# Kernel tuning notes

Hardware: AMD Instinct MI355X
Metric: run time of the kernel (lower is better)

The kernel has to match this reference:

```python
import jax, jax.numpy as jnp
import numpy as np

N = 100000
E = 1600000
DIN = 128
DOUT = 128
NUM_STEPS = 3


def setup_inputs() -> dict:
    key = jax.random.key(0)
    ks = jax.random.split(key, 12)
    stdv = 1.0 / np.sqrt(DOUT)
    xav = np.sqrt(6.0 / (2 * DOUT + DOUT))  # xavier_uniform for [DOUT, 2*DOUT]
    return {
        "input": jax.random.normal(ks[0], (N, DIN), dtype=jnp.float32),
        "edge_row": jax.random.randint(ks[1], (E,), 0, N, dtype=jnp.int32),
        "edge_col": jax.random.randint(ks[2], (E,), 0, N, dtype=jnp.int32),
        "edge_weight": jax.random.uniform(ks[3], (E,), dtype=jnp.float32),
        "weight": jax.random.uniform(ks[4], (DIN, DOUT), jnp.float32, -stdv, stdv),
        "bias": jax.random.uniform(ks[5], (DOUT,), jnp.float32, -stdv, stdv),
        "candidate_weight": jax.random.uniform(ks[6], (DOUT, DOUT), jnp.float32, -stdv, stdv),
        "ug_W": jax.random.uniform(ks[7], (DOUT, 2 * DOUT), jnp.float32, -xav, xav),
        "ug_b": jnp.zeros((DOUT,), jnp.float32),
        "rg_W": jax.random.uniform(ks[8], (DOUT, 2 * DOUT), jnp.float32, -xav, xav),
        "rg_b": jnp.zeros((DOUT,), jnp.float32),
    }


def reference(input, edge_row, edge_col, edge_weight, weight, bias,
              candidate_weight, ug_W, ug_b, rg_W, rg_b):
    n = input.shape[0]
    # h = input @ W + b
    h = input @ weight + bias
    for _ in range(NUM_STEPS):
        # spmm: m[dst] += w_e * h[src]
        msg = edge_weight[:, None] * h[edge_col]          # [E, DOUT]
        m = jax.ops.segment_sum(msg, edge_row, num_segments=n)  # [N, DOUT]
        g = jnp.concatenate([h, m], axis=1)               # [N, 2*DOUT]
        z = jax.nn.sigmoid(g @ ug_W.T + ug_b)
        r = jax.nn.sigmoid(g @ rg_W.T + rg_b)
        cand = jnp.tanh((r * h) @ candidate_weight)
        h = z * h + (1.0 - z) * cand
    return h
```

## Files before the change

### kernel.cpp

```cpp
#include <hip/hip_runtime.h>
#include <math.h>

#define NN 100000
#define EE 1600000
#define D 128
#define NB 782
#define SBLK 98
#define EPB 16384

typedef __attribute__((ext_vector_type(8))) short short8;
typedef __attribute__((ext_vector_type(4))) float floatx4;

static __device__ __forceinline__ unsigned short f2bf(float f) {
  unsigned int u = __builtin_bit_cast(unsigned int, f);
  u = (u + 0x7fff + ((u >> 16) & 1)) >> 16;
  return (unsigned short)u;
}
static __device__ __forceinline__ unsigned int pk2(float a, float b) {
  return (unsigned int)f2bf(a) | ((unsigned int)f2bf(b) << 16);
}
static __device__ __forceinline__ float bflo(unsigned int u) { return __builtin_bit_cast(float, u << 16); }
static __device__ __forceinline__ float bfhi(unsigned int u) { return __builtin_bit_cast(float, u & 0xffff0000u); }
static __device__ __forceinline__ float bf2f(unsigned short s) {
  return __builtin_bit_cast(float, (unsigned int)s << 16);
}
static __device__ __forceinline__ float sig_f(float x) { return 1.f / (1.f + __expf(-x)); }
static __device__ __forceinline__ float tanh_f(float x) {
  float e = __expf(2.f * x);
  return 1.f - 2.f / (e + 1.f);
}


__global__ __launch_bounds__(1024) void b_count(const int* __restrict__ erow, int* __restrict__ cnt_pb) {
  __shared__ int s[NB];
  const int tid = threadIdx.x;
  for (int b = tid; b < NB; b += 1024) s[b] = 0;
  __syncthreads();
  const int base = blockIdx.x * EPB;
#pragma unroll
  for (int i = 0; i < 16; ++i) {
    int idx = base + i * 1024 + tid;
    if (idx < EE) atomicAdd(&s[erow[idx] >> 7], 1);
  }
  __syncthreads();
  for (int b = tid; b < NB; b += 1024) cnt_pb[blockIdx.x * NB + b] = s[b];
}

__global__ __launch_bounds__(1024) void b_scan(const int* __restrict__ cnt_pb,
                                               int* __restrict__ base_pb, int* __restrict__ bucket_off) {
  __shared__ int s[1024];
  const int b = threadIdx.x;
  int tot = 0;
  if (b < NB) {
    for (int j = 0; j < SBLK; ++j) tot += cnt_pb[j * NB + b];
  }
  s[b] = tot;
  __syncthreads();
  for (int d = 1; d < 1024; d <<= 1) {
    int v = (b >= d) ? s[b - d] : 0;
    __syncthreads();
    s[b] += v;
    __syncthreads();
  }
  int excl = s[b] - tot;
  if (b < NB) {
    bucket_off[b] = excl;
    int run = excl;
    for (int j = 0; j < SBLK; ++j) { base_pb[j * NB + b] = run; run += cnt_pb[j * NB + b]; }
  }
  if (b == NB - 1) bucket_off[NB] = excl + tot;
}

__global__ __launch_bounds__(1024) void b_scatter(const int* __restrict__ erow, const int* __restrict__ ecol,
                                                  const float* __restrict__ ew,
                                                  const int* __restrict__ base_pb, int2* __restrict__ arena) {
  __shared__ int cur[NB];
  const int tid = threadIdx.x;
  for (int b = tid; b < NB; b += 1024) cur[b] = base_pb[blockIdx.x * NB + b];
  __syncthreads();
  const int base = blockIdx.x * EPB;
#pragma unroll
  for (int i = 0; i < 16; ++i) {
    int idx = base + i * 1024 + tid;
    if (idx < EE) {
      int r = erow[idx];
      int pos = atomicAdd(&cur[r >> 7], 1);
      int2 v;
      v.x = ecol[idx] | ((r & 127) << 24);
      v.y = __builtin_bit_cast(int, ew[idx]);
      arena[pos] = v;
    }
  }
}

__global__ __launch_bounds__(256) void b_sort(const int* __restrict__ bucket_off, const int2* __restrict__ arena,
                                              int2* __restrict__ edata, int* __restrict__ row_start) {
  __shared__ int rcnt[128];
  __shared__ int rcur[128];
  const int b = blockIdx.x;
  const int tid = threadIdx.x;
  const int lo = bucket_off[b], hi = bucket_off[b + 1];

  if (tid < 128) rcnt[tid] = 0;
  __syncthreads();
  for (int i = lo + tid; i < hi; i += 256) atomicAdd(&rcnt[(arena[i].x >> 24) & 127], 1);
  __syncthreads();
  int myc = (tid < 128) ? rcnt[tid] : 0;
  for (int d = 1; d < 128; d <<= 1) {
    int v = (tid < 128 && tid >= d) ? rcnt[tid - d] : 0;
    __syncthreads();
    if (tid < 128) rcnt[tid] += v;
    __syncthreads();
  }
  if (tid < 128) {
    int excl = rcnt[tid] - myc;
    rcur[tid] = lo + excl;
    int gr = b * 128 + tid;
    if (gr < NN) row_start[gr] = lo + excl;
  }
  if (b == NB - 1 && tid == 0) row_start[NN] = hi;
  __syncthreads();

  for (int i = lo + tid; i < hi; i += 256) {
    int2 v = arena[i];
    int rl = (v.x >> 24) & 127;
    int pos = atomicAdd(&rcur[rl], 1);
    int2 o;
    o.x = v.x & 0x00FFFFFF;
    o.y = v.y;
    edata[pos] = o;
  }
}

__global__ __launch_bounds__(64) void k_pack_zr(const float* __restrict__ ugW, const float* __restrict__ rgW,
                                                unsigned int* __restrict__ packZR) {
  int g = blockIdx.x;
  int nt = g >> 3, ks = g & 7;
  int lane = threadIdx.x;
  int o = nt * 16 + (lane & 15);
  int c0 = ks * 32 + (lane >> 4) * 8;
  const float* src = (o < 128 ? ugW + (size_t)o * 256 : rgW + (size_t)(o - 128) * 256) + c0;
  float4 f0 = ((const float4*)src)[0];
  float4 f1 = ((const float4*)src)[1];
  uint4 out;
  out.x = pk2(f0.x, f0.y);
  out.y = pk2(f0.z, f0.w);
  out.z = pk2(f1.x, f1.y);
  out.w = pk2(f1.z, f1.w);
  ((uint4*)packZR)[g * 64 + lane] = out;
}

__global__ __launch_bounds__(64) void k_pack_kn(const float* __restrict__ M, unsigned int* __restrict__ pack) {
  int g = blockIdx.x;
  int nt = g >> 2, ks = g & 3;
  int lane = threadIdx.x;
  int n = nt * 16 + (lane & 15);
  int k0 = ks * 32 + (lane >> 4) * 8;
  unsigned short v[8];
#pragma unroll
  for (int j = 0; j < 8; ++j) v[j] = f2bf(M[(size_t)(k0 + j) * 128 + n]);
  uint4 out;
  out.x = (unsigned int)v[0] | ((unsigned int)v[1] << 16);
  out.y = (unsigned int)v[2] | ((unsigned int)v[3] << 16);
  out.z = (unsigned int)v[4] | ((unsigned int)v[5] << 16);
  out.w = (unsigned int)v[6] | ((unsigned int)v[7] << 16);
  ((uint4*)pack)[g * 64 + lane] = out;
}

__global__ __launch_bounds__(256) void init_mfma(
    const float* __restrict__ X, const short* __restrict__ packW, const float* __restrict__ bias,
    unsigned short* __restrict__ h_bf) {
  __shared__ __align__(16) short sX[32 * 136];
  const int tid = threadIdx.x;
  const int row0 = blockIdx.x * 32;

  {
    int r = tid >> 3, ch = tid & 7;
    const float4* px = (const float4*)(X + (size_t)(row0 + r) * D + ch * 16);
    float4 f0 = px[0], f1 = px[1], f2 = px[2], f3 = px[3];
    uint4 o0, o1;
    o0.x = pk2(f0.x, f0.y); o0.y = pk2(f0.z, f0.w);
    o0.z = pk2(f1.x, f1.y); o0.w = pk2(f1.z, f1.w);
    o1.x = pk2(f2.x, f2.y); o1.y = pk2(f2.z, f2.w);
    o1.z = pk2(f3.x, f3.y); o1.w = pk2(f3.z, f3.w);
    *(uint4*)(sX + r * 136 + ch * 16) = o0;
    *(uint4*)(sX + r * 136 + ch * 16 + 8) = o1;
  }
  __syncthreads();

  const int wave = tid >> 6, lane = tid & 63;
  const int quad = lane >> 4, l15 = lane & 15;
  const int mh = wave & 1, nh = wave >> 1;
  const int mrow = mh * 16 + l15;

  floatx4 acc[4];
  const floatx4 zero4 = {0.f, 0.f, 0.f, 0.f};
#pragma unroll
  for (int t = 0; t < 4; ++t) acc[t] = zero4;

  const short8* pW = (const short8*)packW;
#pragma unroll
  for (int ks = 0; ks < 4; ++ks) {
    short8 a = *(const short8*)(sX + mrow * 136 + ks * 32 + quad * 8);
#pragma unroll
    for (int t = 0; t < 4; ++t) {
      short8 b = pW[((nh * 4 + t) * 4 + ks) * 64 + lane];
      acc[t] = __builtin_amdgcn_mfma_f32_16x16x32_bf16(a, b, acc[t], 0, 0, 0);
    }
  }

#pragma unroll
  for (int t = 0; t < 4; ++t) {
    int col = nh * 64 + t * 16 + l15;
    float bv = bias[col];
#pragma unroll
    for (int reg = 0; reg < 4; ++reg) {
      int row = mh * 16 + quad * 4 + reg;
      h_bf[(size_t)(row0 + row) * D + col] = f2bf(acc[t][reg] + bv);
    }
  }
}

__global__ __launch_bounds__(512, 8) void fused_step(
    const int* __restrict__ row_start, const int2* __restrict__ edata,
    const uint4* __restrict__ h4,
    const short* __restrict__ packZR, const short* __restrict__ packCW,
    const float* __restrict__ ugb, const float* __restrict__ rgb,
    unsigned short* __restrict__ h_bf_out, float* __restrict__ h_f32_out, int last) {
  __shared__ __align__(16) short sA[32 * 264];
  __shared__ __align__(16) short sRH[32 * 136];

  const int tid = threadIdx.x;
  const int row0 = blockIdx.x * 32;
  const int wave = tid >> 6, lane = tid & 63;
  const int sub = lane >> 4, li = lane & 15;

  {
    int r = tid >> 4, ch = tid & 15;
    *(uint4*)(sA + r * 264 + ch * 8) = h4[(size_t)(row0 + r) * 16 + ch];
  }

  {
    const int rbase = row0 + wave * 4;
    int rs[5];
#pragma unroll
    for (int j = 0; j < 5; ++j) rs[j] = row_start[rbase + j];

    for (int i = 0; i < 4; ++i) {
      const int s0 = rs[i], end = rs[i + 1];
      float acc[8];
#pragma unroll
      for (int j = 0; j < 8; ++j) acc[j] = 0.f;

      int kk = s0;
      for (; kk + 8 <= end; kk += 8) {
        int2 e0 = edata[kk + sub];
        int2 e1 = edata[kk + 4 + sub];
        uint4 h0 = h4[(size_t)e0.x * 16 + li];
        uint4 h1 = h4[(size_t)e1.x * 16 + li];
        float w0 = __builtin_bit_cast(float, e0.y);
        float w1 = __builtin_bit_cast(float, e1.y);
        acc[0] += w0 * bflo(h0.x); acc[1] += w0 * bfhi(h0.x);
        acc[2] += w0 * bflo(h0.y); acc[3] += w0 * bfhi(h0.y);
        acc[4] += w0 * bflo(h0.z); acc[5] += w0 * bfhi(h0.z);
        acc[6] += w0 * bflo(h0.w); acc[7] += w0 * bfhi(h0.w);
        acc[0] += w1 * bflo(h1.x); acc[1] += w1 * bfhi(h1.x);
        acc[2] += w1 * bflo(h1.y); acc[3] += w1 * bfhi(h1.y);
        acc[4] += w1 * bflo(h1.z); acc[5] += w1 * bfhi(h1.z);
        acc[6] += w1 * bflo(h1.w); acc[7] += w1 * bfhi(h1.w);
      }
      for (; kk < end; kk += 4) {
        int e = kk + sub;
        if (e < end) {
          int2 ed = edata[e];
          uint4 hv = h4[(size_t)ed.x * 16 + li];
          float w = __builtin_bit_cast(float, ed.y);
          acc[0] += w * bflo(hv.x); acc[1] += w * bfhi(hv.x);
          acc[2] += w * bflo(hv.y); acc[3] += w * bfhi(hv.y);
          acc[4] += w * bflo(hv.z); acc[5] += w * bfhi(hv.z);
          acc[6] += w * bflo(hv.w); acc[7] += w * bfhi(hv.w);
        }
      }

#pragma unroll
      for (int j = 0; j < 8; ++j) acc[j] += __shfl_xor(acc[j], 16, 64);
#pragma unroll
      for (int j = 0; j < 8; ++j) acc[j] += __shfl_xor(acc[j], 32, 64);

      if (sub == 0) {
        int rl = wave * 4 + i;
        uint4 o;
        o.x = pk2(acc[0], acc[1]);
        o.y = pk2(acc[2], acc[3]);
        o.z = pk2(acc[4], acc[5]);
        o.w = pk2(acc[6], acc[7]);
        *(uint4*)(sA + rl * 264 + 128 + li * 8) = o;
      }
    }
  }
  __syncthreads();

  const int quad = lane >> 4, l15 = lane & 15;
  const int mh = wave >> 2, nh = wave & 3;
  const int mrow = mh * 16 + l15;

  floatx4 accZ[2], accR[2];
  const floatx4 zero4 = {0.f, 0.f, 0.f, 0.f};
#pragma unroll
  for (int t = 0; t < 2; ++t) { accZ[t] = zero4; accR[t] = zero4; }

  const short8* pB = (const short8*)packZR;
#pragma unroll
  for (int ks = 0; ks < 8; ++ks) {
    short8 a = *(const short8*)(sA + mrow * 264 + ks * 32 + quad * 8);
#pragma unroll
    for (int t = 0; t < 2; ++t) {
      short8 bz = pB[((nh * 2 + t) * 8 + ks) * 64 + lane];
      accZ[t] = __builtin_amdgcn_mfma_f32_16x16x32_bf16(a, bz, accZ[t], 0, 0, 0);
      short8 br = pB[((8 + nh * 2 + t) * 8 + ks) * 64 + lane];
      accR[t] = __builtin_amdgcn_mfma_f32_16x16x32_bf16(a, br, accR[t], 0, 0, 0);
    }
  }

#pragma unroll
  for (int t = 0; t < 2; ++t) {
    int col = nh * 32 + t * 16 + l15;
    float zb = ugb[col], rb = rgb[col];
#pragma unroll
    for (int reg = 0; reg < 4; ++reg) {
      int row = mh * 16 + quad * 4 + reg;
      float z = sig_f(accZ[t][reg] + zb);
      float rr = sig_f(accR[t][reg] + rb);
      float hv = bf2f((unsigned short)sA[row * 264 + col]);
      sRH[row * 136 + col] = (short)f2bf(rr * hv);
      accZ[t][reg] = z;
    }
  }
  __syncthreads();

  floatx4 acc2[2];
#pragma unroll
  for (int t = 0; t < 2; ++t) acc2[t] = zero4;

  const short8* pC = (const short8*)packCW;
#pragma unroll
  for (int ks = 0; ks < 4; ++ks) {
    short8 a = *(const short8*)(sRH + mrow * 136 + ks * 32 + quad * 8);
#pragma unroll
    for (int t = 0; t < 2; ++t) {
      short8 b = pC[((nh * 2 + t) * 4 + ks) * 64 + lane];
      acc2[t] = __builtin_amdgcn_mfma_f32_16x16x32_bf16(a, b, acc2[t], 0, 0, 0);
    }
  }

#pragma unroll
  for (int t = 0; t < 2; ++t) {
    int col = nh * 32 + t * 16 + l15;
#pragma unroll
    for (int reg = 0; reg < 4; ++reg) {
      int row = mh * 16 + quad * 4 + reg;
      float cand = tanh_f(acc2[t][reg]);
      float z = accZ[t][reg];
      float hold = bf2f((unsigned short)sA[row * 264 + col]);
      float hn = z * hold + (1.f - z) * cand;
      size_t gi = (size_t)(row0 + row) * D + col;
      if (last) h_f32_out[gi] = hn;
      else h_bf_out[gi] = f2bf(hn);
    }
  }
}

extern "C" void kernel_launch(void* const* d_in, const int* in_sizes, int n_in,
                              void* d_out, int out_size, void* d_ws, size_t ws_size,
                              hipStream_t stream) {
  const float* input = (const float*)d_in[0];
  const int* erow    = (const int*)d_in[1];
  const int* ecol    = (const int*)d_in[2];
  const float* ew    = (const float*)d_in[3];
  const float* W     = (const float*)d_in[4];
  const float* bias  = (const float*)d_in[5];
  const float* CW    = (const float*)d_in[6];
  const float* ugW   = (const float*)d_in[7];
  const float* ugb   = (const float*)d_in[8];
  const float* rgW   = (const float*)d_in[9];
  const float* rgb   = (const float*)d_in[10];

  float* h_out = (float*)d_out;

  char* ws = (char*)d_ws;
  unsigned short* hA = (unsigned short*)ws;   ws += (size_t)NN * D * 2;
  unsigned short* hB = (unsigned short*)ws;   ws += (size_t)NN * D * 2;
  unsigned int* packZR = (unsigned int*)ws;   ws += 16 * 8 * 64 * 16;
  unsigned int* packCW = (unsigned int*)ws;   ws += 8 * 4 * 64 * 16;
  unsigned int* packW  = (unsigned int*)ws;   ws += 8 * 4 * 64 * 16;
  int2* arena    = (int2*)ws;                 ws += (size_t)EE * sizeof(int2);
  int2* edata    = (int2*)ws;                 ws += (size_t)EE * sizeof(int2);
  int* cnt_pb    = (int*)ws;                  ws += SBLK * NB * sizeof(int);
  int* base_pb   = (int*)ws;                  ws += SBLK * NB * sizeof(int);
  int* bucket_off= (int*)ws;                  ws += (NB + 1) * sizeof(int);
  int* row_start = (int*)ws;                  ws += (NN + 1) * sizeof(int);

  b_count<<<SBLK, 1024, 0, stream>>>(erow, cnt_pb);
  b_scan<<<1, 1024, 0, stream>>>(cnt_pb, base_pb, bucket_off);
  b_scatter<<<SBLK, 1024, 0, stream>>>(erow, ecol, ew, base_pb, arena);
  b_sort<<<NB, 256, 0, stream>>>(bucket_off, arena, edata, row_start);

  k_pack_zr<<<128, 64, 0, stream>>>(ugW, rgW, packZR);
  k_pack_kn<<<32, 64, 0, stream>>>(CW, packCW);
  k_pack_kn<<<32, 64, 0, stream>>>(W, packW);
  init_mfma<<<NN / 32, 256, 0, stream>>>(input, (const short*)packW, bias, hA);

  fused_step<<<NN / 32, 512, 0, stream>>>(row_start, edata, (const uint4*)hA,
                                          (const short*)packZR, (const short*)packCW,
                                          ugb, rgb, hB, h_out, 0);
  fused_step<<<NN / 32, 512, 0, stream>>>(row_start, edata, (const uint4*)hB,
                                          (const short*)packZR, (const short*)packCW,
                                          ugb, rgb, hA, h_out, 0);
  fused_step<<<NN / 32, 512, 0, stream>>>(row_start, edata, (const uint4*)hA,
                                          (const short*)packZR, (const short*)packCW,
                                          ugb, rgb, hB, h_out, 1);
}
```

Measured before the change: 529.4 us.

## Stage edge chunks in LDS, assign one row per quarter-wave, coalesce output stores

The SpMM gather now loads each block's contiguous edge range into shared memory in chunks, and each 16-lane group handles a single row, so no cross-lane shuffle reduction is needed. Output writes in init and fused_step go through shared memory and are stored as 16-byte coalesced rows instead of scattered 2-byte stores. The bucketing kernels use 256-thread blocks over 4x more blocks, and their count buffers are placed in the h workspace that is not yet used. The cost is extra barriers and the LDS reuse for sRH, and a row's edges are processed serially by 16 lanes, which hurts when degrees vary.

Result: no change. 530.3 us (+0.2%).

```diff
diff --git a/kernel.cpp b/kernel.cpp
--- a/kernel.cpp
+++ b/kernel.cpp
@@ -5,8 +5,9 @@
 #define EE 1600000
 #define D 128
 #define NB 782
-#define SBLK 98
-#define EPB 16384
+#define SBLK 392
+#define EPB 4096
+#define EMAX 2048
 
 typedef __attribute__((ext_vector_type(8))) short short8;
 typedef __attribute__((ext_vector_type(4))) float floatx4;
@@ -29,21 +30,27 @@
   float e = __expf(2.f * x);
   return 1.f - 2.f / (e + 1.f);
 }
-
-
-__global__ __launch_bounds__(1024) void b_count(const int* __restrict__ erow, int* __restrict__ cnt_pb) {
+static __device__ __forceinline__ void fma8(float* acc, float w, uint4 h) {
+  acc[0] += w * bflo(h.x); acc[1] += w * bfhi(h.x);
+  acc[2] += w * bflo(h.y); acc[3] += w * bfhi(h.y);
+  acc[4] += w * bflo(h.z); acc[5] += w * bfhi(h.z);
+  acc[6] += w * bflo(h.w); acc[7] += w * bfhi(h.w);
+}
+
+
+__global__ __launch_bounds__(256) void b_count(const int* __restrict__ erow, int* __restrict__ cnt_pb) {
   __shared__ int s[NB];
   const int tid = threadIdx.x;
-  for (int b = tid; b < NB; b += 1024) s[b] = 0;
+  for (int b = tid; b < NB; b += 256) s[b] = 0;
   __syncthreads();
   const int base = blockIdx.x * EPB;
 #pragma unroll
   for (int i = 0; i < 16; ++i) {
-    int idx = base + i * 1024 + tid;
+    int idx = base + i * 256 + tid;
     if (idx < EE) atomicAdd(&s[erow[idx] >> 7], 1);
   }
   __syncthreads();
-  for (int b = tid; b < NB; b += 1024) cnt_pb[blockIdx.x * NB + b] = s[b];
+  for (int b = tid; b < NB; b += 256) cnt_pb[blockIdx.x * NB + b] = s[b];
 }
 
 __global__ __launch_bounds__(1024) void b_scan(const int* __restrict__ cnt_pb,
@@ -71,17 +78,17 @@
   if (b == NB - 1) bucket_off[NB] = excl + tot;
 }
 
-__global__ __launch_bounds__(1024) void b_scatter(const int* __restrict__ erow, const int* __restrict__ ecol,
+__global__ __launch_bounds__(256) void b_scatter(const int* __restrict__ erow, const int* __restrict__ ecol,
                                                   const float* __restrict__ ew,
                                                   const int* __restrict__ base_pb, int2* __restrict__ arena) {
   __shared__ int cur[NB];
   const int tid = threadIdx.x;
-  for (int b = tid; b < NB; b += 1024) cur[b] = base_pb[blockIdx.x * NB + b];
+  for (int b = tid; b < NB; b += 256) cur[b] = base_pb[blockIdx.x * NB + b];
   __syncthreads();
   const int base = blockIdx.x * EPB;
 #pragma unroll
   for (int i = 0; i < 16; ++i) {
-    int idx = base + i * 1024 + tid;
+    int idx = base + i * 256 + tid;
     if (idx < EE) {
       int r = erow[idx];
       int pos = atomicAdd(&cur[r >> 7], 1);
@@ -209,6 +216,7 @@
     }
   }
 
+  __syncthreads();
 #pragma unroll
   for (int t = 0; t < 4; ++t) {
     int col = nh * 64 + t * 16 + l15;
@@ -216,8 +224,13 @@
 #pragma unroll
     for (int reg = 0; reg < 4; ++reg) {
       int row = mh * 16 + quad * 4 + reg;
-      h_bf[(size_t)(row0 + row) * D + col] = f2bf(acc[t][reg] + bv);
-    }
+      sX[row * 136 + col] = (short)f2bf(acc[t][reg] + bv);
+    }
+  }
+  __syncthreads();
+  for (int idx = tid; idx < 512; idx += 256) {
+    int r = idx >> 4, ch = idx & 15;
+    *(uint4*)(h_bf + (size_t)(row0 + r) * D + ch * 8) = *(uint4*)(sX + r * 136 + ch * 8);
   }
 }
 
@@ -228,7 +241,9 @@
     const float* __restrict__ ugb, const float* __restrict__ rgb,
     unsigned short* __restrict__ h_bf_out, float* __restrict__ h_f32_out, int last) {
   __shared__ __align__(16) short sA[32 * 264];
-  __shared__ __align__(16) short sRH[32 * 136];
+  __shared__ __align__(16) char sU[EMAX * 8];
+  int2* sE = (int2*)sU;
+  short* sRH = (short*)sU;
 
   const int tid = threadIdx.x;
   const int row0 = blockIdx.x * 32;
@@ -240,63 +255,46 @@
     *(uint4*)(sA + r * 264 + ch * 8) = h4[(size_t)(row0 + r) * 16 + ch];
   }
 
+  const int myrow = row0 + wave * 4 + sub;
+  const int rs0 = row_start[myrow];
+  const int rs1 = row_start[myrow + 1];
+  const int seg_lo = row_start[row0];
+  const int seg_hi = row_start[row0 + 32];
+
+  float acc[8];
+#pragma unroll
+  for (int j = 0; j < 8; ++j) acc[j] = 0.f;
+
+  for (int clo = seg_lo; clo < seg_hi; clo += EMAX) {
+    const int chi = min(clo + EMAX, seg_hi);
+    for (int i = clo + tid; i < chi; i += 512) sE[i - clo] = edata[i];
+    __syncthreads();
+
+    int kb = max(rs0, clo) - clo;
+    int ke = min(rs1, chi) - clo;
+    for (; kb + 2 <= ke; kb += 2) {
+      int2 e0 = sE[kb];
+      int2 e1 = sE[kb + 1];
+      uint4 h0 = h4[(size_t)e0.x * 16 + li];
+      uint4 h1 = h4[(size_t)e1.x * 16 + li];
+      fma8(acc, __builtin_bit_cast(float, e0.y), h0);
+      fma8(acc, __builtin_bit_cast(float, e1.y), h1);
+    }
+    if (kb < ke) {
+      int2 e0 = sE[kb];
+      uint4 h0 = h4[(size_t)e0.x * 16 + li];
+      fma8(acc, __builtin_bit_cast(float, e0.y), h0);
+    }
+    __syncthreads();
+  }
+
   {
-    const int rbase = row0 + wave * 4;
-    int rs[5];
-#pragma unroll
-    for (int j = 0; j < 5; ++j) rs[j] = row_start[rbase + j];
-
-    for (int i = 0; i < 4; ++i) {
-      const int s0 = rs[i], end = rs[i + 1];
-      float acc[8];
-#pragma unroll
-      for (int j = 0; j < 8; ++j) acc[j] = 0.f;
-
-      int kk = s0;
-      for (; kk + 8 <= end; kk += 8) {
-        int2 e0 = edata[kk + sub];
-        int2 e1 = edata[kk + 4 + sub];
-        uint4 h0 = h4[(size_t)e0.x * 16 + li];
-        uint4 h1 = h4[(size_t)e1.x * 16 + li];
-        float w0 = __builtin_bit_cast(float, e0.y);
-        float w1 = __builtin_bit_cast(float, e1.y);
-        acc[0] += w0 * bflo(h0.x); acc[1] += w0 * bfhi(h0.x);
-        acc[2] += w0 * bflo(h0.y); acc[3] += w0 * bfhi(h0.y);
-        acc[4] += w0 * bflo(h0.z); acc[5] += w0 * bfhi(h0.z);
-        acc[6] += w0 * bflo(h0.w); acc[7] += w0 * bfhi(h0.w);
-        acc[0] += w1 * bflo(h1.x); acc[1] += w1 * bfhi(h1.x);
-        acc[2] += w1 * bflo(h1.y); acc[3] += w1 * bfhi(h1.y);
-        acc[4] += w1 * bflo(h1.z); acc[5] += w1 * bfhi(h1.z);
-        acc[6] += w1 * bflo(h1.w); acc[7] += w1 * bfhi(h1.w);
-      }
-      for (; kk < end; kk += 4) {
-        int e = kk + sub;
-        if (e < end) {
-          int2 ed = edata[e];
-          uint4 hv = h4[(size_t)ed.x * 16 + li];
-          float w = __builtin_bit_cast(float, ed.y);
-          acc[0] += w * bflo(hv.x); acc[1] += w * bfhi(hv.x);
-          acc[2] += w * bflo(hv.y); acc[3] += w * bfhi(hv.y);
-          acc[4] += w * bflo(hv.z); acc[5] += w * bfhi(hv.z);
-          acc[6] += w * bflo(hv.w); acc[7] += w * bfhi(hv.w);
-        }
-      }
-
-#pragma unroll
-      for (int j = 0; j < 8; ++j) acc[j] += __shfl_xor(acc[j], 16, 64);
-#pragma unroll
-      for (int j = 0; j < 8; ++j) acc[j] += __shfl_xor(acc[j], 32, 64);
-
-      if (sub == 0) {
-        int rl = wave * 4 + i;
-        uint4 o;
-        o.x = pk2(acc[0], acc[1]);
-        o.y = pk2(acc[2], acc[3]);
-        o.z = pk2(acc[4], acc[5]);
-        o.w = pk2(acc[6], acc[7]);
-        *(uint4*)(sA + rl * 264 + 128 + li * 8) = o;
-      }
-    }
+    uint4 o;
+    o.x = pk2(acc[0], acc[1]);
+    o.y = pk2(acc[2], acc[3]);
+    o.z = pk2(acc[4], acc[5]);
+    o.w = pk2(acc[6], acc[7]);
+    *(uint4*)(sA + (wave * 4 + sub) * 264 + 128 + li * 8) = o;
   }
   __syncthreads();
 
@@ -363,10 +361,14 @@
       float z = accZ[t][reg];
       float hold = bf2f((unsigned short)sA[row * 264 + col]);
       float hn = z * hold + (1.f - z) * cand;
-      size_t gi = (size_t)(row0 + row) * D + col;
-      if (last) h_f32_out[gi] = hn;
-      else h_bf_out[gi] = f2bf(hn);
-    }
+      if (last) h_f32_out[(size_t)(row0 + row) * D + col] = hn;
+      else sA[row * 264 + col] = (short)f2bf(hn);
+    }
+  }
+  if (!last) {
+    __syncthreads();
+    int r = tid >> 4, ch = tid & 15;
+    *(uint4*)(h_bf_out + (size_t)(row0 + r) * D + ch * 8) = *(uint4*)(sA + r * 264 + ch * 8);
   }
 }
 
@@ -395,14 +397,14 @@
   unsigned int* packW  = (unsigned int*)ws;   ws += 8 * 4 * 64 * 16;
   int2* arena    = (int2*)ws;                 ws += (size_t)EE * sizeof(int2);
   int2* edata    = (int2*)ws;                 ws += (size_t)EE * sizeof(int2);
-  int* cnt_pb    = (int*)ws;                  ws += SBLK * NB * sizeof(int);
-  int* base_pb   = (int*)ws;                  ws += SBLK * NB * sizeof(int);
   int* bucket_off= (int*)ws;                  ws += (NB + 1) * sizeof(int);
   int* row_start = (int*)ws;                  ws += (NN + 1) * sizeof(int);
-
-  b_count<<<SBLK, 1024, 0, stream>>>(erow, cnt_pb);
+  int* cnt_pb  = (int*)hA;
+  int* base_pb = (int*)((char*)hA + (size_t)SBLK * NB * sizeof(int));
+
+  b_count<<<SBLK, 256, 0, stream>>>(erow, cnt_pb);
   b_scan<<<1, 1024, 0, stream>>>(cnt_pb, base_pb, bucket_off);
-  b_scatter<<<SBLK, 1024, 0, stream>>>(erow, ecol, ew, base_pb, arena);
+  b_scatter<<<SBLK, 256, 0, stream>>>(erow, ecol, ew, base_pb, arena);
   b_sort<<<NB, 256, 0, stream>>>(bucket_off, arena, edata, row_start);
 
   k_pack_zr<<<128, 64, 0, stream>>>(ugW, rgW, packZR);
```
